# Kernel tuning notes

Hardware: AMD Instinct MI355X
Metric: run time of the kernel (lower is better)

Reference implementation:

```python
import jax, jax.numpy as jnp
import numpy as np

K = 32          # neighbors
DIV = 4         # division
S = K // DIV    # maxpool window
EPS = 1e-5      # BatchNorm eps (torch default)


def _bn_last(x, g, b):
    # BatchNorm over channel = last axis, training-mode batch stats (biased var),
    # equivalent to torch's transpose->BatchNorm2d->transpose in Dense(in_dim=4).
    m = x.mean(axis=(0, 1, 2), keepdims=True)
    v = x.var(axis=(0, 1, 2), keepdims=True)
    return (x - m) / jnp.sqrt(v + EPS) * g + b


def setup_inputs() -> dict:
    key = jax.random.key(0)
    ks = jax.random.split(key, 16)
    B, N, M, F1, F2 = 8, 4096, 2048, 128, 256
    Fmid = 64
    Cin = Fmid + F1  # 192
    inp = {
        "points": jax.random.normal(ks[0], (B, N, 3), dtype=jnp.float32),
        "queries": jax.random.normal(ks[1], (B, M, 3), dtype=jnp.float32),
        "prev_features": jax.random.normal(ks[2], (B, N, F1), dtype=jnp.float32),
        # dense1: 3 -> 32
        "g1": jnp.ones((3,), jnp.float32),
        "b1": jnp.zeros((3,), jnp.float32),
        "W1": jax.random.normal(ks[3], (3, Fmid // 2), dtype=jnp.float32) * 0.3,
        "c1": jnp.zeros((Fmid // 2,), jnp.float32),
        # dense2: 32 -> 64
        "g2": jnp.ones((Fmid // 2,), jnp.float32),
        "b2": jnp.zeros((Fmid // 2,), jnp.float32),
        "W2": jax.random.normal(ks[4], (Fmid // 2, Fmid), dtype=jnp.float32) * 0.1,
        "c2": jnp.zeros((Fmid,), jnp.float32),
        # conv block: BN2d(192) + Conv2d(192 -> 256, kernel (1,4))
        "g3": jnp.ones((Cin,), jnp.float32),
        "b3": jnp.zeros((Cin,), jnp.float32),
        "Wc": jax.random.normal(ks[5], (F2, Cin, DIV), dtype=jnp.float32) * 0.05,
        "bc": jnp.zeros((F2,), jnp.float32),
    }
    return inp


def reference(points, queries, prev_features, g1, b1, W1, c1, g2, b2, W2, c2,
              g3, b3, Wc, bc):
    B, N, _ = points.shape
    M = queries.shape[1]

    # --- KNN: negative squared distance, topk largest = k nearest ---
    # dist[b,m,n] = -||q-p||^2 = 2 q.p - ||q||^2 - ||p||^2
    dist = (2.0 * jnp.einsum('bmd,bnd->bmn', queries, points)
            - jnp.sum(queries ** 2, -1)[:, :, None]
            - jnp.sum(points ** 2, -1)[:, None, :])
    _, idx = jax.lax.top_k(dist, K)  # (B, M, K) int32

    gather = jax.vmap(lambda feats, i: feats[i])  # (N,F),(M,K) -> (M,K,F)
    knn_pts = gather(points, idx)                 # (B, M, K, 3)

    # local coords: center - neighbor
    local = queries[:, :, None, :] - knn_pts       # (B, M, K, 3)

    # dense1 / dense2: BN -> Linear -> ReLU
    h = jax.nn.relu(_bn_last(local, g1, b1) @ W1 + c1)  # (B,M,K,32)
    h = jax.nn.relu(_bn_last(h, g2, b2) @ W2 + c2)      # (B,M,K,64)

    # gather previous features, concat
    prev_k = gather(prev_features, idx)                 # (B,M,K,F1)
    feat = jnp.concatenate([h, prev_k], axis=-1)        # (B,M,K,192)

    # permute to NCHW, maxpool (1,S) stride S over K -> width DIV
    x = jnp.transpose(feat, (0, 3, 1, 2))               # (B,C,M,K)
    C = x.shape[1]
    x = x.reshape(B, C, M, DIV, S).max(axis=-1)         # (B,C,M,DIV)

    # BN2d over channel (training-mode batch stats)
    m = x.mean(axis=(0, 2, 3), keepdims=True)
    v = x.var(axis=(0, 2, 3), keepdims=True)
    x = (x - m) / jnp.sqrt(v + EPS) * g3[None, :, None, None] + b3[None, :, None, None]

    # Conv2d kernel (1,DIV) collapses width to 1: contraction over (C, DIV)
    out = jnp.einsum('bcmd,ocd->bmo', x, Wc) + bc       # (B,M,F2)
    return jax.nn.relu(out)
```

## Files before the change

### kernel.cpp

```cpp
#include <hip/hip_runtime.h>
#include <hip/hip_bf16.h>
#include <math.h>


#define B_   8
#define N_   4096
#define M_   2048
#define K_   32
#define F1_  128
#define F2_  256
#define CIN_ 192
#define NROWS_ (B_*M_*K_)
#define NQ_    (B_*M_)
#define EPS_ 1e-5f

#define S2_BLK 64
#define S3_BLK 512

typedef __attribute__((ext_vector_type(8))) short bf16x8;
typedef __attribute__((ext_vector_type(4))) float f32x4;

__device__ __forceinline__ unsigned int fkey(float qx, float qy, float qz, float qq,
                                             float x, float y, float z) {
    float dot = fmaf(qz, z, fmaf(qy, y, __fmul_rn(qx, x)));
    float pp  = __fadd_rn(__fadd_rn(__fmul_rn(x, x), __fmul_rn(y, y)), __fmul_rn(z, z));
    float d   = __fsub_rn(__fsub_rn(__fmul_rn(2.0f, dot), qq), pp);
    unsigned int u = __float_as_uint(d);
    return u ^ ((unsigned int)((int)u >> 31) | 0x80000000u);
}

__device__ __forceinline__ unsigned int pack_hi(float f0, float f1) {
    return (__float_as_uint(f0) >> 16) | (__float_as_uint(f1) & 0xFFFF0000u);
}
__device__ __forceinline__ unsigned int pack_lo(float f0, float f1) {
    float r0 = f0 - __uint_as_float(__float_as_uint(f0) & 0xFFFF0000u);
    float r1 = f1 - __uint_as_float(__float_as_uint(f1) & 0xFFFF0000u);
    return (__float_as_uint(r0) >> 16) | (__float_as_uint(r1) & 0xFFFF0000u);
}

__global__ __launch_bounds__(512) void knn_kernel(const float* __restrict__ points,
                                                  const float* __restrict__ queries,
                                                  int* __restrict__ idx_out,
                                                  float* __restrict__ local_out,
                                                  float* __restrict__ part1) {
    __shared__ float px[4160], py[4160], pz[4160];
    __shared__ float acc1[8][6];
    const int q0 = blockIdx.x * 8;
    const int b  = q0 >> 11;
    const float* pb = points + (size_t)b * N_ * 3;
    for (int p = threadIdx.x; p < N_; p += 512) {
        const float* g = pb + p * 3;
        int a = (p >> 6) * 65 + (p & 63);
        px[a] = g[0]; py[a] = g[1]; pz[a] = g[2];
    }
    __syncthreads();

    const int lane = threadIdx.x & 63;
    const int wid  = threadIdx.x >> 6;
    const int q = q0 + wid;
    const float qx = queries[q * 3 + 0];
    const float qy = queries[q * 3 + 1];
    const float qz = queries[q * 3 + 2];
    const float qq = __fadd_rn(__fadd_rn(__fmul_rn(qx, qx), __fmul_rn(qy, qy)), __fmul_rn(qz, qz));

    unsigned int m_fk = 0u, bj = 0u;
    #pragma unroll 8
    for (unsigned int j = 0; j < 64; ++j) {
        int a = (int)j * 65 + lane;
        unsigned int fk = fkey(qx, qy, qz, qq, px[a], py[a], pz[a]);
        if (fk > m_fk) { m_fk = fk; bj = j; }
    }
    unsigned int m_n = (unsigned int)lane + (bj << 6);

    unsigned long long takenT = 0ull;
    int sel_n = 0;
    const int rb = lane * 65;
    for (int r = 0; r < 32; ++r) {
        unsigned int g = m_fk;
        #pragma unroll
        for (int off = 32; off; off >>= 1) {
            unsigned int o = __shfl_xor(g, off, 64);
            g = (o > g) ? o : g;
        }
        unsigned long long mk = __ballot(m_fk == g);
        unsigned int nstar;
        if (__popcll(mk) == 1) {
            int src = __ffsll(mk) - 1;
            nstar = (unsigned int)__shfl((int)m_n, src, 64);
        } else {
            unsigned int nm = (m_fk == g) ? m_n : 0xFFFFFFFFu;
            #pragma unroll
            for (int off = 32; off; off >>= 1) {
                unsigned int o = __shfl_xor(nm, off, 64);
                nm = (o < nm) ? o : nm;
            }
            nstar = nm;
        }
        if (lane == r) sel_n = (int)nstar;
        const int w  = nstar & 63;
        const int js = (int)(nstar >> 6);
        if (lane == js) takenT |= (1ull << w);
        int a2 = rb + w;
        unsigned int fk2 = fkey(qx, qy, qz, qq, px[a2], py[a2], pz[a2]);
        if ((unsigned int)(takenT >> w) & 1u) fk2 = 0u;
        unsigned int g2 = fk2;
        #pragma unroll
        for (int off = 32; off; off >>= 1) {
            unsigned int o = __shfl_xor(g2, off, 64);
            g2 = (o > g2) ? o : g2;
        }
        unsigned long long mk2 = __ballot(fk2 == g2);
        int src2 = __ffsll(mk2) - 1;
        if (lane == w) { m_fk = g2; m_n = (unsigned int)(w + (src2 << 6)); }
    }

    float vx = 0.f, vy = 0.f, vz = 0.f;
    if (lane < 32) {
        idx_out[q * K_ + lane] = sel_n;
        int a = (sel_n >> 6) * 65 + (sel_n & 63);
        vx = __fsub_rn(qx, px[a]);
        vy = __fsub_rn(qy, py[a]);
        vz = __fsub_rn(qz, pz[a]);
        size_t o = ((size_t)q * K_ + lane) * 3;
        local_out[o + 0] = vx; local_out[o + 1] = vy; local_out[o + 2] = vz;
    }
    float s0 = vx, s1 = vy, s2 = vz, s3 = vx*vx, s4 = vy*vy, s5 = vz*vz;
    #pragma unroll
    for (int off = 32; off; off >>= 1) {
        s0 += __shfl_xor(s0, off, 64); s1 += __shfl_xor(s1, off, 64);
        s2 += __shfl_xor(s2, off, 64); s3 += __shfl_xor(s3, off, 64);
        s4 += __shfl_xor(s4, off, 64); s5 += __shfl_xor(s5, off, 64);
    }
    if (lane == 0) { acc1[wid][0]=s0; acc1[wid][1]=s1; acc1[wid][2]=s2;
                     acc1[wid][3]=s3; acc1[wid][4]=s4; acc1[wid][5]=s5; }
    __syncthreads();
    if (threadIdx.x < 6) {
        float s = 0.f;
        #pragma unroll
        for (int i = 0; i < 8; ++i) s += acc1[i][threadIdx.x];
        part1[blockIdx.x * 8 + threadIdx.x] = s;
    }
}

__global__ __launch_bounds__(256) void fold1_kernel(const float* __restrict__ part1,
                             const float* __restrict__ g1, const float* __restrict__ b1,
                             const float* __restrict__ W1, const float* __restrict__ c1,
                             float* __restrict__ W1p, float* __restrict__ c1p) {
    __shared__ float red[32][8];
    __shared__ float cs[8];
    const int t = threadIdx.x;
    const int c = t & 7, ch = t >> 3;
    float s = 0.f;
    for (int i = 0; i < 64; ++i) s += part1[(ch * 64 + i) * 8 + c];
    red[ch][c] = s;
    __syncthreads();
    if (t < 8) {
        float v = 0.f;
        #pragma unroll
        for (int i = 0; i < 32; ++i) v += red[i][t];
        cs[t] = v;
    }
    __syncthreads();
    if (t >= 32) return;
    const float inv_n = 1.0f / (float)NROWS_;
    float cacc = c1[t];
    #pragma unroll
    for (int c3 = 0; c3 < 3; ++c3) {
        float mean = cs[c3] * inv_n;
        float var  = cs[3 + c3] * inv_n - mean * mean;
        float sc   = g1[c3] / sqrtf(var + EPS_);
        float tc   = b1[c3] - mean * sc;
        float w    = W1[c3 * 32 + t];
        W1p[c3 * 32 + t] = sc * w;
        cacc += tc * w;
    }
    c1p[t] = cacc;
}

__global__ __launch_bounds__(256) void stats2_kernel(const float* __restrict__ local,
                                                     const float* __restrict__ W1p,
                                                     const float* __restrict__ c1p,
                                                     float* __restrict__ part2) {
    __shared__ float w[96], cb[32];
    __shared__ float red[4][64];
    if (threadIdx.x < 96) w[threadIdx.x] = W1p[threadIdx.x];
    if (threadIdx.x < 32) cb[threadIdx.x] = c1p[threadIdx.x];
    __syncthreads();
    float sum[32], sq[32];
    #pragma unroll
    for (int i = 0; i < 32; ++i) { sum[i] = 0.f; sq[i] = 0.f; }
    int tid = blockIdx.x * 256 + threadIdx.x;
    for (int r = tid; r < NROWS_; r += S2_BLK * 256) {
        float x = local[(size_t)r*3], y = local[(size_t)r*3+1], z = local[(size_t)r*3+2];
        #pragma unroll
        for (int f = 0; f < 32; ++f) {
            float h = fmaf(z, w[64 + f], fmaf(y, w[32 + f], fmaf(x, w[f], cb[f])));
            h = fmaxf(h, 0.0f);
            sum[f] += h; sq[f] += h * h;
        }
    }
    #pragma unroll
    for (int f = 0; f < 32; ++f) {
        #pragma unroll
        for (int off = 32; off; off >>= 1) {
            sum[f] += __shfl_xor(sum[f], off, 64);
            sq[f]  += __shfl_xor(sq[f], off, 64);
        }
    }
    int lane = threadIdx.x & 63, wid = threadIdx.x >> 6;
    if (lane == 0) {
        #pragma unroll
        for (int f = 0; f < 32; ++f) { red[wid][f] = sum[f]; red[wid][32 + f] = sq[f]; }
    }
    __syncthreads();
    if (threadIdx.x < 64) {
        part2[blockIdx.x * 64 + threadIdx.x] =
            red[0][threadIdx.x] + red[1][threadIdx.x] + red[2][threadIdx.x] + red[3][threadIdx.x];
    }
}

__global__ void fold2_kernel(const float* __restrict__ part2,
                             const float* __restrict__ g2, const float* __restrict__ b2,
                             const float* __restrict__ W2, const float* __restrict__ c2,
                             float* __restrict__ W2p, float* __restrict__ c2p) {
    __shared__ float cs[64];
    int f = threadIdx.x;
    {
        float s = 0.f;
        for (int i = 0; i < S2_BLK; ++i) s += part2[i * 64 + f];
        cs[f] = s;
    }
    __syncthreads();
    const float inv_n = 1.0f / (float)NROWS_;
    float cacc = c2[f];
    for (int c = 0; c < 32; ++c) {
        float mean = cs[c] * inv_n;
        float var  = cs[32 + c] * inv_n - mean * mean;
        float sc   = g2[c] / sqrtf(var + EPS_);
        float tc   = b2[c] - mean * sc;
        float wv   = W2[c * 64 + f];
        W2p[c * 64 + f] = sc * wv;
        cacc += tc * wv;
    }
    c2p[f] = cacc;
}

__global__ __launch_bounds__(256) void h2pool_kernel(const float* __restrict__ local,
                                                     const float* __restrict__ W1p,
                                                     const float* __restrict__ c1p,
                                                     const float* __restrict__ W2p,
                                                     const float* __restrict__ c2p,
                                                     float* __restrict__ xp) {
    __shared__ float h1buf[4][32 * 32];
    const int lane = threadIdx.x & 63, wid = threadIdx.x >> 6;
    const int q = blockIdx.x * 4 + wid;

    float w2c[32];
    #pragma unroll 8
    for (int c = 0; c < 32; ++c) w2c[c] = W2p[c * 64 + lane];
    const float c2l = c2p[lane];

    const int f0 = lane & 31;
    const float wa = W1p[f0], wb = W1p[32 + f0], wc = W1p[64 + f0], cc = c1p[f0];
    float* hb = &h1buf[wid][0];
    #pragma unroll 2
    for (int i = 0; i < 16; ++i) {
        int t = lane + 64 * i;
        int k = t >> 5;
        size_t lo = ((size_t)q * K_ + k) * 3;
        float x = local[lo], y = local[lo + 1], z = local[lo + 2];
        float h = fmaf(z, wc, fmaf(y, wb, fmaf(x, wa, cc)));
        hb[t] = fmaxf(h, 0.0f);
    }
    __syncthreads();

    float pm[4] = {-INFINITY, -INFINITY, -INFINITY, -INFINITY};
    #pragma unroll 2
    for (int k = 0; k < 32; ++k) {
        const float* hk = &hb[k * 32];
        float acc = c2l;
        #pragma unroll
        for (int c = 0; c < 32; ++c) acc = fmaf(hk[c], w2c[c], acc);
        float h2 = fmaxf(acc, 0.0f);
        int g = k >> 3;
        pm[g] = fmaxf(pm[g], h2);
    }

    float* xq = xp + (size_t)q * 4 * CIN_;
    #pragma unroll
    for (int g = 0; g < 4; ++g) xq[g * CIN_ + lane] = pm[g];
}

__global__ __launch_bounds__(256) void gatherpool_kernel(const int* __restrict__ idx,
                                                         const float* __restrict__ prev,
                                                         float* __restrict__ xp) {
    const int lane = threadIdx.x & 63, wid = threadIdx.x >> 6;
    const int bid = blockIdx.x;
    const int q = ((bid & 7) << 11) + ((bid >> 3) << 2) + wid;
    const int b = q >> 11;

    int iv = 0;
    if (lane < 32) iv = idx[q * K_ + lane];
    float p0[4] = {-INFINITY, -INFINITY, -INFINITY, -INFINITY};
    float p1[4] = {-INFINITY, -INFINITY, -INFINITY, -INFINITY};
    const float* pbase = prev + (size_t)b * N_ * F1_;
    #pragma unroll 4
    for (int k = 0; k < 32; ++k) {
        int row = __shfl(iv, k, 64);
        const float* pr = pbase + (size_t)row * F1_;
        float v0 = pr[lane];
        float v1 = pr[64 + lane];
        int g = k >> 3;
        p0[g] = fmaxf(p0[g], v0);
        p1[g] = fmaxf(p1[g], v1);
    }

    float* xq = xp + (size_t)q * 4 * CIN_;
    #pragma unroll
    for (int g = 0; g < 4; ++g) {
        xq[g * CIN_ + 64 + lane]  = p0[g];
        xq[g * CIN_ + 128 + lane] = p1[g];
    }
}

__global__ __launch_bounds__(192) void stats3_kernel(const float* __restrict__ xp,
                                                     float* __restrict__ part3) {
    int c = threadIdx.x;
    int r0 = blockIdx.x * 128;
    float s = 0.f, sq = 0.f;
    #pragma unroll 4
    for (int i = 0; i < 128; ++i) {
        float v = xp[(size_t)(r0 + i) * CIN_ + c];
        s += v; sq += v * v;
    }
    part3[blockIdx.x * 384 + c]       = s;
    part3[blockIdx.x * 384 + 192 + c] = sq;
}

__global__ __launch_bounds__(384) void finalize3_kernel(const float* __restrict__ part3,
                                                        float* __restrict__ stats3) {
    int t = threadIdx.x;
    float s = 0.f;
    for (int i = 0; i < S3_BLK; ++i) s += part3[i * 384 + t];
    stats3[t] = s;
}

__global__ __launch_bounds__(256) void fold3_kernel(const float* __restrict__ stats3,
                                                    const float* __restrict__ g3, const float* __restrict__ b3,
                                                    const float* __restrict__ Wc, const float* __restrict__ bc,
                                                    unsigned short* __restrict__ Wh,
                                                    unsigned short* __restrict__ Wl,
                                                    float* __restrict__ bcp) {
    const int o = blockIdx.x;
    const float inv_n = 1.0f / (float)(NQ_ * 4);
    __shared__ float red[256];
    float tacc = 0.f;
    for (int t = threadIdx.x; t < CIN_ * 4; t += 256) {
        int c = t >> 2, d = t & 3;
        float mean = stats3[c] * inv_n;
        float var  = stats3[192 + c] * inv_n - mean * mean;
        float sc   = g3[c] / sqrtf(var + EPS_);
        float tc   = b3[c] - mean * sc;
        float wv   = Wc[(size_t)o * (CIN_ * 4) + t];
        float w    = sc * wv;
        unsigned int u = __float_as_uint(w);
        float rr = w - __uint_as_float(u & 0xFFFF0000u);
        int f  = d * CIN_ + c;
        int ks = f >> 5, j = f & 7, lg = (f >> 3) & 3;
        size_t fi = ((size_t)(ks * 16 + (o >> 4)) * 64 + (lg * 16 + (o & 15))) * 8 + j;
        Wh[fi] = (unsigned short)(u >> 16);
        Wl[fi] = (unsigned short)(__float_as_uint(rr) >> 16);
        tacc += tc * wv;
    }
    red[threadIdx.x] = tacc;
    __syncthreads();
    for (int s = 128; s; s >>= 1) {
        if (threadIdx.x < s) red[threadIdx.x] += red[threadIdx.x + s];
        __syncthreads();
    }
    if (threadIdx.x == 0) bcp[o] = bc[o] + red[0];
}

__global__ __launch_bounds__(512) void conv_kernel(const float* __restrict__ xp,
                                                   const unsigned short* __restrict__ Wh,
                                                   const unsigned short* __restrict__ Wl,
                                                   const float* __restrict__ bcp,
                                                   float* __restrict__ out) {
    __shared__ __align__(16) unsigned short Ah_s[64 * 64];
    __shared__ __align__(16) unsigned short Al_s[64 * 64];
    __shared__ __align__(16) unsigned short Bh_s[2 * 16 * 64 * 8];
    __shared__ __align__(16) unsigned short Bl_s[2 * 16 * 64 * 8];

    const int tid  = threadIdx.x;
    const int lane = tid & 63;
    const int wid  = tid >> 6;
    const int wr   = wid >> 2;
    const int wc   = wid & 3;
    const int row0 = blockIdx.x * 64;

    f32x4 acc[2][4];
    #pragma unroll
    for (int i = 0; i < 2; ++i)
        #pragma unroll
        for (int n = 0; n < 4; ++n) acc[i][n] = (f32x4){0.f, 0.f, 0.f, 0.f};

    const int ar  = tid >> 3;
    const int akq = tid & 7;
    const int a_byte = ar * 128 + ((akq ^ (ar & 7)) << 4);
    const float* arow = xp + (size_t)(row0 + ar) * 768 + akq * 8;

    const int fr_row = lane & 15;
    const int fr_grp = lane >> 4;

    for (int ks2 = 0; ks2 < 12; ++ks2) {
        __syncthreads();
        {
            const float* p = arow + ks2 * 64;
            float4 v0 = *(const float4*)p;
            float4 v1 = *(const float4*)(p + 4);
            uint4 h4, l4;
            h4.x = pack_hi(v0.x, v0.y); h4.y = pack_hi(v0.z, v0.w);
            h4.z = pack_hi(v1.x, v1.y); h4.w = pack_hi(v1.z, v1.w);
            l4.x = pack_lo(v0.x, v0.y); l4.y = pack_lo(v0.z, v0.w);
            l4.z = pack_lo(v1.x, v1.y); l4.w = pack_lo(v1.z, v1.w);
            *(uint4*)((char*)Ah_s + a_byte) = h4;
            *(uint4*)((char*)Al_s + a_byte) = l4;
        }
        {
            const uint4* gh = (const uint4*)(Wh + (size_t)ks2 * 16384);
            const uint4* gl = (const uint4*)(Wl + (size_t)ks2 * 16384);
            uint4* lh = (uint4*)Bh_s;
            uint4* ll = (uint4*)Bl_s;
            #pragma unroll
            for (int i = 0; i < 4; ++i) {
                lh[tid + 512 * i] = gh[tid + 512 * i];
                ll[tid + 512 * i] = gl[tid + 512 * i];
            }
        }
        __syncthreads();
        #pragma unroll
        for (int ks = 0; ks < 2; ++ks) {
            bf16x8 ah[2], al[2];
            #pragma unroll
            for (int i = 0; i < 2; ++i) {
                int r = wr * 32 + i * 16 + fr_row;
                int slot = ks * 4 + fr_grp;
                int byte = r * 128 + ((slot ^ (r & 7)) << 4);
                ah[i] = *(const bf16x8*)((const char*)Ah_s + byte);
                al[i] = *(const bf16x8*)((const char*)Al_s + byte);
            }
            #pragma unroll
            for (int nt = 0; nt < 4; ++nt) {
                int bidx = ((ks * 16 + wc * 4 + nt) * 64 + lane) * 8;
                bf16x8 bh = *(const bf16x8*)(Bh_s + bidx);
                bf16x8 bl = *(const bf16x8*)(Bl_s + bidx);
                #pragma unroll
                for (int i = 0; i < 2; ++i) {
                    acc[i][nt] = __builtin_amdgcn_mfma_f32_16x16x32_bf16(ah[i], bh, acc[i][nt], 0, 0, 0);
                    acc[i][nt] = __builtin_amdgcn_mfma_f32_16x16x32_bf16(ah[i], bl, acc[i][nt], 0, 0, 0);
                    acc[i][nt] = __builtin_amdgcn_mfma_f32_16x16x32_bf16(al[i], bh, acc[i][nt], 0, 0, 0);
                }
            }
        }
    }

    float bias[4];
    #pragma unroll
    for (int nt = 0; nt < 4; ++nt) bias[nt] = bcp[wc * 64 + nt * 16 + fr_row];
    #pragma unroll
    for (int i = 0; i < 2; ++i) {
        #pragma unroll
        for (int nt = 0; nt < 4; ++nt) {
            int col = wc * 64 + nt * 16 + fr_row;
            #pragma unroll
            for (int rg = 0; rg < 4; ++rg) {
                int row = row0 + wr * 32 + i * 16 + fr_grp * 4 + rg;
                out[(size_t)row * F2_ + col] = fmaxf(acc[i][nt][rg] + bias[nt], 0.0f);
            }
        }
    }
}

extern "C" void kernel_launch(void* const* d_in, const int* in_sizes, int n_in,
                              void* d_out, int out_size, void* d_ws, size_t ws_size,
                              hipStream_t stream) {
    const float* points  = (const float*)d_in[0];
    const float* queries = (const float*)d_in[1];
    const float* prev    = (const float*)d_in[2];
    const float* g1 = (const float*)d_in[3];
    const float* b1 = (const float*)d_in[4];
    const float* W1 = (const float*)d_in[5];
    const float* c1 = (const float*)d_in[6];
    const float* g2 = (const float*)d_in[7];
    const float* b2 = (const float*)d_in[8];
    const float* W2 = (const float*)d_in[9];
    const float* c2 = (const float*)d_in[10];
    const float* g3 = (const float*)d_in[11];
    const float* b3 = (const float*)d_in[12];
    const float* Wc = (const float*)d_in[13];
    const float* bc = (const float*)d_in[14];
    float* out = (float*)d_out;

    char* ws = (char*)d_ws;
    size_t off_idx    = 0;
    size_t off_local  = off_idx + (size_t)NQ_*K_*4;
    size_t off_stats3 = off_local + (size_t)NROWS_*3*4;
    size_t off_W1p    = off_stats3 + 4096;
    size_t off_c1p    = off_W1p + 512;
    size_t off_W2p    = off_c1p + 512;
    size_t off_c2p    = off_W2p + 8192;
    size_t off_Wt     = off_c2p + 512;
    size_t off_bcp    = off_Wt + 786432;
    size_t off_xp     = off_bcp + 1024;

    int*   idx    = (int*)(ws + off_idx);
    float* local  = (float*)(ws + off_local);
    float* stats3 = (float*)(ws + off_stats3);
    float* W1p    = (float*)(ws + off_W1p);
    float* c1p    = (float*)(ws + off_c1p);
    float* W2p    = (float*)(ws + off_W2p);
    float* c2p    = (float*)(ws + off_c2p);
    unsigned short* Wh = (unsigned short*)(ws + off_Wt);
    unsigned short* Wl = (unsigned short*)(ws + off_Wt + 393216);
    float* bcp    = (float*)(ws + off_bcp);
    float* xp     = (float*)(ws + off_xp);
    float* part1  = (float*)(ws + off_Wt);
    float* part2  = (float*)(ws + off_Wt + 65536);
    float* part3  = (float*)(ws + off_local);

    knn_kernel<<<NQ_ / 8, 512, 0, stream>>>(points, queries, idx, local, part1);
    fold1_kernel<<<1, 256, 0, stream>>>(part1, g1, b1, W1, c1, W1p, c1p);
    stats2_kernel<<<S2_BLK, 256, 0, stream>>>(local, W1p, c1p, part2);
    fold2_kernel<<<1, 64, 0, stream>>>(part2, g2, b2, W2, c2, W2p, c2p);
    h2pool_kernel<<<NQ_ / 4, 256, 0, stream>>>(local, W1p, c1p, W2p, c2p, xp);
    gatherpool_kernel<<<NQ_ / 4, 256, 0, stream>>>(idx, prev, xp);
    stats3_kernel<<<S3_BLK, 192, 0, stream>>>(xp, part3);
    finalize3_kernel<<<1, 384, 0, stream>>>(part3, stats3);
    fold3_kernel<<<F2_, 256, 0, stream>>>(stats3, g3, b3, Wc, bc, Wh, Wl, bcp);
    conv_kernel<<<NQ_ / 64, 512, 0, stream>>>(xp, Wh, Wl, bcp, out);
}
```

Before: 416.2 us.

## Track top-2 per lane in KNN, widen stats2 grid, tweak unrolls

The KNN selection now keeps the two best candidates per lane column, so after a lane's best is taken the second best is promoted and the column is only rescanned when both are used up. This removes most of the per-round fkey rescans and shuffle reductions. Separately, stats2 runs 512 blocks instead of 64, fold2 reduces the partials with two halves across 128 threads, gather and finalize loops get more unrolling, and fkey fuses the multiply-subtract into an fma. The fma can change distance rounding and so tie order in top-k. The larger stats2 grid also needs part2 to fit its workspace slot.

```diff
diff --git a/kernel.cpp b/kernel.cpp
--- a/kernel.cpp
+++ b/kernel.cpp
@@ -14,7 +14,7 @@
 #define NQ_    (B_*M_)
 #define EPS_ 1e-5f
 
-#define S2_BLK 64
+#define S2_BLK 512
 #define S3_BLK 512
 
 typedef __attribute__((ext_vector_type(8))) short bf16x8;
@@ -24,7 +24,7 @@
                                              float x, float y, float z) {
     float dot = fmaf(qz, z, fmaf(qy, y, __fmul_rn(qx, x)));
     float pp  = __fadd_rn(__fadd_rn(__fmul_rn(x, x), __fmul_rn(y, y)), __fmul_rn(z, z));
-    float d   = __fsub_rn(__fsub_rn(__fmul_rn(2.0f, dot), qq), pp);
+    float d   = __fsub_rn(fmaf(2.0f, dot, -qq), pp);
     unsigned int u = __float_as_uint(d);
     return u ^ ((unsigned int)((int)u >> 31) | 0x80000000u);
 }
@@ -63,32 +63,37 @@
     const float qz = queries[q * 3 + 2];
     const float qq = __fadd_rn(__fadd_rn(__fmul_rn(qx, qx), __fmul_rn(qy, qy)), __fmul_rn(qz, qz));
 
-    unsigned int m_fk = 0u, bj = 0u;
+    unsigned int fk0 = 0u, fk1 = 0u, n0 = 0u, n1 = 0u;
+    unsigned int n = (unsigned int)lane;
     #pragma unroll 8
-    for (unsigned int j = 0; j < 64; ++j) {
-        int a = (int)j * 65 + lane;
+    for (int j = 0; j < 64; ++j) {
+        int a = j * 65 + lane;
         unsigned int fk = fkey(qx, qy, qz, qq, px[a], py[a], pz[a]);
-        if (fk > m_fk) { m_fk = fk; bj = j; }
-    }
-    unsigned int m_n = (unsigned int)lane + (bj << 6);
+        if (fk > fk1) {
+            bool g0 = fk > fk0;
+            fk1 = g0 ? fk0 : fk;  n1 = g0 ? n0 : n;
+            fk0 = g0 ? fk  : fk0; n0 = g0 ? n  : n0;
+        }
+        n += 64u;
+    }
 
     unsigned long long takenT = 0ull;
     int sel_n = 0;
     const int rb = lane * 65;
     for (int r = 0; r < 32; ++r) {
-        unsigned int g = m_fk;
+        unsigned int g = fk0;
         #pragma unroll
         for (int off = 32; off; off >>= 1) {
             unsigned int o = __shfl_xor(g, off, 64);
             g = (o > g) ? o : g;
         }
-        unsigned long long mk = __ballot(m_fk == g);
+        unsigned long long mk = __ballot(fk0 == g);
         unsigned int nstar;
         if (__popcll(mk) == 1) {
             int src = __ffsll(mk) - 1;
-            nstar = (unsigned int)__shfl((int)m_n, src, 64);
+            nstar = (unsigned int)__shfl((int)n0, src, 64);
         } else {
-            unsigned int nm = (m_fk == g) ? m_n : 0xFFFFFFFFu;
+            unsigned int nm = (fk0 == g) ? n0 : 0xFFFFFFFFu;
             #pragma unroll
             for (int off = 32; off; off >>= 1) {
                 unsigned int o = __shfl_xor(nm, off, 64);
@@ -100,18 +105,22 @@
         const int w  = nstar & 63;
         const int js = (int)(nstar >> 6);
         if (lane == js) takenT |= (1ull << w);
-        int a2 = rb + w;
-        unsigned int fk2 = fkey(qx, qy, qz, qq, px[a2], py[a2], pz[a2]);
-        if ((unsigned int)(takenT >> w) & 1u) fk2 = 0u;
-        unsigned int g2 = fk2;
-        #pragma unroll
-        for (int off = 32; off; off >>= 1) {
-            unsigned int o = __shfl_xor(g2, off, 64);
-            g2 = (o > g2) ? o : g2;
-        }
-        unsigned long long mk2 = __ballot(fk2 == g2);
-        int src2 = __ffsll(mk2) - 1;
-        if (lane == w) { m_fk = g2; m_n = (unsigned int)(w + (src2 << 6)); }
+        if (lane == w) { fk0 = fk1; n0 = n1; fk1 = 0u; }
+        unsigned long long need = __ballot(lane == w && fk0 == 0u);
+        if (need) {
+            int a2 = rb + w;
+            unsigned int fk2 = fkey(qx, qy, qz, qq, px[a2], py[a2], pz[a2]);
+            if ((unsigned int)(takenT >> w) & 1u) fk2 = 0u;
+            unsigned int g2 = fk2;
+            #pragma unroll
+            for (int off = 32; off; off >>= 1) {
+                unsigned int o = __shfl_xor(g2, off, 64);
+                g2 = (o > g2) ? o : g2;
+            }
+            unsigned long long mk2 = __ballot(fk2 == g2);
+            int src2 = __ffsll(mk2) - 1;
+            if (lane == w) { fk0 = g2; n0 = (unsigned int)w + ((unsigned int)src2 << 6); }
+        }
     }
 
     float vx = 0.f, vy = 0.f, vz = 0.f;
@@ -223,13 +232,20 @@
                              const float* __restrict__ g2, const float* __restrict__ b2,
                              const float* __restrict__ W2, const float* __restrict__ c2,
                              float* __restrict__ W2p, float* __restrict__ c2p) {
+    __shared__ float red2[2][64];
     __shared__ float cs[64];
-    int f = threadIdx.x;
+    int t = threadIdx.x;
+    int f = t & 63, h = t >> 6;
     {
         float s = 0.f;
-        for (int i = 0; i < S2_BLK; ++i) s += part2[i * 64 + f];
-        cs[f] = s;
-    }
+        #pragma unroll 8
+        for (int i = h * (S2_BLK / 2); i < (h + 1) * (S2_BLK / 2); ++i)
+            s += part2[i * 64 + f];
+        red2[h][f] = s;
+    }
+    __syncthreads();
+    if (t >= 64) return;
+    cs[f] = red2[0][f] + red2[1][f];
     __syncthreads();
     const float inv_n = 1.0f / (float)NROWS_;
     float cacc = c2[f];
@@ -304,7 +320,7 @@
     float p0[4] = {-INFINITY, -INFINITY, -INFINITY, -INFINITY};
     float p1[4] = {-INFINITY, -INFINITY, -INFINITY, -INFINITY};
     const float* pbase = prev + (size_t)b * N_ * F1_;
-    #pragma unroll 4
+    #pragma unroll 8
     for (int k = 0; k < 32; ++k) {
         int row = __shfl(iv, k, 64);
         const float* pr = pbase + (size_t)row * F1_;
@@ -341,6 +357,7 @@
                                                         float* __restrict__ stats3) {
     int t = threadIdx.x;
     float s = 0.f;
+    #pragma unroll 4
     for (int i = 0; i < S3_BLK; ++i) s += part3[i * 384 + t];
     stats3[t] = s;
 }
@@ -531,7 +548,7 @@
     knn_kernel<<<NQ_ / 8, 512, 0, stream>>>(points, queries, idx, local, part1);
     fold1_kernel<<<1, 256, 0, stream>>>(part1, g1, b1, W1, c1, W1p, c1p);
     stats2_kernel<<<S2_BLK, 256, 0, stream>>>(local, W1p, c1p, part2);
-    fold2_kernel<<<1, 64, 0, stream>>>(part2, g2, b2, W2, c2, W2p, c2p);
+    fold2_kernel<<<1, 128, 0, stream>>>(part2, g2, b2, W2, c2, W2p, c2p);
     h2pool_kernel<<<NQ_ / 4, 256, 0, stream>>>(local, W1p, c1p, W2p, c2p, xp);
     gatherpool_kernel<<<NQ_ / 4, 256, 0, stream>>>(idx, prev, xp);
     stats3_kernel<<<S3_BLK, 192, 0, stream>>>(xp, part3);
```

New measurement: 405.2 us. -2.6%, faster.
